# Kernel tuning notes

Measured on AMD Instinct MI355X. Metric: run time of the kernel, lower is better.

Reference implementation:

```python
import jax, jax.numpy as jnp
import numpy as np

THRESHOLD = 1.0
NEG_SLOPE = 0.2
N_NODES = 100000
N_EDGES = 1600000
DIM = 64
N_LAYERS = 3


def setup_inputs() -> dict:
    key = jax.random.key(0)
    ks = jax.random.split(key, 6)
    x = jax.random.normal(ks[0], (N_NODES, DIM), dtype=jnp.float32)
    edge_index = jax.random.randint(ks[1], (2, N_EDGES), 0, N_NODES, dtype=jnp.int64)
    scale = 1.0 / np.sqrt(DIM)
    W = jax.random.normal(ks[2], (N_LAYERS, DIM, DIM), dtype=jnp.float32) * scale
    a_src = jax.random.normal(ks[3], (N_LAYERS, DIM), dtype=jnp.float32) * scale
    a_dst = jax.random.normal(ks[4], (N_LAYERS, DIM), dtype=jnp.float32) * scale
    b = jnp.zeros((N_LAYERS, DIM), dtype=jnp.float32)
    return {"x": x, "edge_index": edge_index, "W": W, "a_src": a_src, "a_dst": a_dst, "b": b}


def reference(x, edge_index, W, a_src, a_dst, b):
    N = x.shape[0]
    # GATConv default add_self_loops=True: append (i -> i) for every node
    self_loop = jnp.arange(N, dtype=edge_index.dtype)
    src = jnp.concatenate([edge_index[0], self_loop])  # message source j
    dst = jnp.concatenate([edge_index[1], self_loop])  # message target i

    h = x
    for l in range(W.shape[0]):
        hw = h @ W[l]                       # [N, d] linear transform
        alpha_s = hw @ a_src[l]             # [N] per-node src attention logits
        alpha_d = hw @ a_dst[l]             # [N] per-node dst attention logits
        e = jax.nn.leaky_relu(alpha_s[src] + alpha_d[dst], NEG_SLOPE)  # [E']
        # softmax over incoming edges of each dst node (segment softmax)
        m = jax.ops.segment_max(e, dst, num_segments=N)
        p = jnp.exp(e - m[dst])
        s = jax.ops.segment_sum(p, dst, num_segments=N)
        attn = p / s[dst]
        out = jax.ops.segment_sum(attn[:, None] * hw[src], dst, num_segments=N)
        h = jnp.clip(out + b[l], -THRESHOLD, THRESHOLD)  # act_fn = clamp
    return h
```

## Files before the change

kernel.cpp:

```cpp
#include <hip/hip_runtime.h>
#include <hip/hip_fp16.h>

#define NN 100000
#define NE 1600000
#define DIM 64
#define NL 3
#define SLOPE 0.2f

#define BSH 9
#define NBUCK ((NN + 511) >> BSH)
#define EPT 16
#define TILE (256 * EPT)
#define MT 128

static __device__ __forceinline__ float lrelu(float x) { return x > 0.f ? x : SLOPE * x; }

static __device__ __forceinline__ float4 load_h4(const ushort* __restrict__ base, size_t off) {
    uint2 u = *(const uint2*)(base + off);
    __half2 h0 = __builtin_bit_cast(__half2, u.x);
    __half2 h1 = __builtin_bit_cast(__half2, u.y);
    float2 f0 = __half22float2(h0);
    float2 f1 = __half22float2(h1);
    return make_float4(f0.x, f0.y, f1.x, f1.y);
}


__global__ __launch_bounds__(256) void k_bucket_hist(const int* __restrict__ ei, int* __restrict__ bcnt) {
    __shared__ int h[256];
    int t = threadIdx.x;
    h[t] = 0;
    __syncthreads();
    for (int e = blockIdx.x * 256 + t; e < NE; e += 256 * 256) atomicAdd(&h[ei[NE + e] >> BSH], 1);
    __syncthreads();
    if (t < NBUCK && h[t]) atomicAdd(&bcnt[t], h[t]);
}

__global__ void k_bucket_scan(const int* __restrict__ bcnt, int* __restrict__ bbase, int* __restrict__ bcur,
                              int* __restrict__ offs) {
    __shared__ int sm[256];
    int t = threadIdx.x;
    sm[t] = (t < NBUCK) ? bcnt[t] : 0;
    __syncthreads();
    for (int off = 1; off < 256; off <<= 1) {
        int x = (t >= off) ? sm[t - off] : 0;
        __syncthreads();
        sm[t] += x;
        __syncthreads();
    }
    if (t < NBUCK) {
        int ex = (t == 0) ? 0 : sm[t - 1];
        bbase[t] = ex;
        bcur[t] = ex;
    }
    if (t == 0) {
        bbase[NBUCK] = NE;
        offs[NN] = NE;
    }
}

__global__ __launch_bounds__(256) void k_partition(const int* __restrict__ ei, int* __restrict__ bcur,
                                                   int2* __restrict__ pairs) {
    __shared__ int2 tile[TILE];
    __shared__ int cnt[256], ofsx[256], gdel[256], sm[256];
    int t = threadIdx.x;
    int ts = blockIdx.x * TILE;
    int tilecnt = NE - ts;
    if (tilecnt > TILE) tilecnt = TILE;
    cnt[t] = 0;
    __syncthreads();
    int srcv[EPT], dstv[EPT], rk[EPT];
#pragma unroll
    for (int k = 0; k < EPT; k++) {
        int e = ts + k * 256 + t;
        if (e < NE) {
            srcv[k] = ei[e];
            dstv[k] = ei[NE + e];
            rk[k] = atomicAdd(&cnt[dstv[k] >> BSH], 1);
        } else {
            rk[k] = -1;
        }
    }
    __syncthreads();
    sm[t] = cnt[t];
    __syncthreads();
    for (int off = 1; off < 256; off <<= 1) {
        int x = (t >= off) ? sm[t - off] : 0;
        __syncthreads();
        sm[t] += x;
        __syncthreads();
    }
    ofsx[t] = (t == 0) ? 0 : sm[t - 1];
    __syncthreads();
#pragma unroll
    for (int k = 0; k < EPT; k++) {
        if (rk[k] >= 0) tile[ofsx[dstv[k] >> BSH] + rk[k]] = make_int2(srcv[k], dstv[k]);
    }
    if (t < NBUCK && cnt[t]) gdel[t] = atomicAdd(&bcur[t], cnt[t]) - ofsx[t];
    __syncthreads();
    for (int i = t; i < tilecnt; i += 256) {
        int2 p = tile[i];
        pairs[gdel[p.y >> BSH] + i] = p;
    }
}

__global__ __launch_bounds__(256) void k_node_csr(const int2* __restrict__ pairs, const int* __restrict__ bbase,
                                                  int* __restrict__ offs, int* __restrict__ csr) {
    __shared__ int deg[512], sofs[512], scur[512], sm[256];
    int t = threadIdx.x;
    int b = blockIdx.x;
    int nodeBase = b << BSH;
    int nNodes = NN - nodeBase;
    if (nNodes > 512) nNodes = 512;
    deg[t] = 0;
    deg[t + 256] = 0;
    __syncthreads();
    int ebeg = bbase[b], eend = bbase[b + 1];
    for (int i = ebeg + t; i < eend; i += 256) atomicAdd(&deg[pairs[i].y - nodeBase], 1);
    __syncthreads();
    int a0 = deg[2 * t], a1 = deg[2 * t + 1];
    sm[t] = a0 + a1;
    __syncthreads();
    for (int off = 1; off < 256; off <<= 1) {
        int x = (t >= off) ? sm[t - off] : 0;
        __syncthreads();
        sm[t] += x;
        __syncthreads();
    }
    int base = (t == 0) ? 0 : sm[t - 1];
    sofs[2 * t] = base;
    sofs[2 * t + 1] = base + a0;
    scur[2 * t] = 0;
    scur[2 * t + 1] = 0;
    __syncthreads();
    for (int n = t; n < nNodes; n += 256) offs[nodeBase + n] = ebeg + sofs[n];
    for (int i = ebeg + t; i < eend; i += 256) {
        int2 p = pairs[i];
        int ln = p.y - nodeBase;
        int r = atomicAdd(&scur[ln], 1);
        csr[ebeg + sofs[ln] + r] = p.x;
    }
}


__global__ __launch_bounds__(256) void k_transform(const float* __restrict__ h, const float* __restrict__ W,
                                                   const float* __restrict__ avs, const float* __restrict__ avd,
                                                   ushort* __restrict__ hw, float* __restrict__ als,
                                                   float* __restrict__ ald) {
    __shared__ float sh[MT][65];
    __shared__ float sw[64][64];
    int t = threadIdx.x;
    int tx = t & 15, ty = t >> 4;
    int base = blockIdx.x * MT;
    int rows = NN - base;
    if (rows > MT) rows = MT;
    {
        const float4* Wv = (const float4*)W;
        float4* swv = (float4*)sw;
        for (int i = t; i < 1024; i += 256) swv[i] = Wv[i];
    }
    for (int i = t; i < MT * 16; i += 256) {
        int r = i >> 4, cs = i & 15;
        float4 v = (r < rows) ? *(const float4*)(h + (size_t)(base + r) * 64 + cs * 4)
                              : make_float4(0.f, 0.f, 0.f, 0.f);
        sh[r][cs * 4 + 0] = v.x;
        sh[r][cs * 4 + 1] = v.y;
        sh[r][cs * 4 + 2] = v.z;
        sh[r][cs * 4 + 3] = v.w;
    }
    __syncthreads();
    float acc[8][4] = {};
    int r0 = ty * 8;
#pragma unroll 4
    for (int k = 0; k < 64; k++) {
        float4 b = *(const float4*)(&sw[k][tx * 4]);
#pragma unroll
        for (int r = 0; r < 8; r++) {
            float a = sh[r0 + r][k];
            acc[r][0] = fmaf(a, b.x, acc[r][0]);
            acc[r][1] = fmaf(a, b.y, acc[r][1]);
            acc[r][2] = fmaf(a, b.z, acc[r][2]);
            acc[r][3] = fmaf(a, b.w, acc[r][3]);
        }
    }
    float4 as4 = *(const float4*)(avs + tx * 4);
    float4 ad4 = *(const float4*)(avd + tx * 4);
#pragma unroll
    for (int r = 0; r < 8; r++) {
        int row = r0 + r;
        bool ok = row < rows;
        if (ok) {
            __half2 h0 = __floats2half2_rn(acc[r][0], acc[r][1]);
            __half2 h1 = __floats2half2_rn(acc[r][2], acc[r][3]);
            uint2 u;
            u.x = __builtin_bit_cast(unsigned int, h0);
            u.y = __builtin_bit_cast(unsigned int, h1);
            *(uint2*)(hw + (size_t)(base + row) * 64 + tx * 4) = u;
        }
        float ps = acc[r][0] * as4.x + acc[r][1] * as4.y + acc[r][2] * as4.z + acc[r][3] * as4.w;
        float pd = acc[r][0] * ad4.x + acc[r][1] * ad4.y + acc[r][2] * ad4.z + acc[r][3] * ad4.w;
#pragma unroll
        for (int off = 1; off <= 8; off <<= 1) {
            ps += __shfl_xor(ps, off);
            pd += __shfl_xor(pd, off);
        }
        if (tx == 0 && ok) {
            als[base + row] = ps;
            ald[base + row] = pd;
        }
    }
}

__global__ __launch_bounds__(256) void k_aggregate(const ushort* __restrict__ hw, const float* __restrict__ als,
                                                   const float* __restrict__ ald, const int* __restrict__ offs,
                                                   const int* __restrict__ csr, const float* __restrict__ bv,
                                                   float* __restrict__ out) {
    int t = threadIdx.x, wave = t >> 6, lane = t & 63;
    int i = blockIdx.x * 4 + wave;
    if (i >= NN) return;
    int q = lane >> 4, c = lane & 15;
    float ad = ald[i];
    float eself = lrelu(als[i] + ad);
    float m = eself;
    float s = 0.f;
    float4 acc = make_float4(0.f, 0.f, 0.f, 0.f);
    int beg = offs[i], end = offs[i + 1];
    for (int cb = beg; cb < end; cb += 64) {
        int cnt = end - cb;
        if (cnt > 64) cnt = 64;
        int src = 0;
        float e = -1e30f;
        if (lane < cnt) {
            src = csr[cb + lane];
            e = lrelu(als[src] + ad);
        }
        float cm = e;
#pragma unroll
        for (int off = 32; off; off >>= 1) cm = fmaxf(cm, __shfl_xor(cm, off));
        float mn = fmaxf(m, cm);
        float p = (lane < cnt) ? __expf(e - mn) : 0.f;
        float cs = p;
#pragma unroll
        for (int off = 32; off; off >>= 1) cs += __shfl_xor(cs, off);
        float sc = __expf(m - mn);
        s = fmaf(s, sc, cs);
        acc.x *= sc;
        acc.y *= sc;
        acc.z *= sc;
        acc.w *= sc;
        m = mn;
        int steps = (cnt + 15) >> 4;
        for (int st = 0; st < steps; st++) {
            int jb = st * 16 + q;
            int s0 = __shfl(src, jb);
            int s1 = __shfl(src, jb + 4);
            int s2 = __shfl(src, jb + 8);
            int s3 = __shfl(src, jb + 12);
            float p0 = __shfl(p, jb);
            float p1 = __shfl(p, jb + 4);
            float p2 = __shfl(p, jb + 8);
            float p3 = __shfl(p, jb + 12);
            float4 v0 = load_h4(hw, (size_t)s0 * 64 + c * 4);
            float4 v1 = load_h4(hw, (size_t)s1 * 64 + c * 4);
            float4 v2 = load_h4(hw, (size_t)s2 * 64 + c * 4);
            float4 v3 = load_h4(hw, (size_t)s3 * 64 + c * 4);
            acc.x = fmaf(p0, v0.x, acc.x);
            acc.y = fmaf(p0, v0.y, acc.y);
            acc.z = fmaf(p0, v0.z, acc.z);
            acc.w = fmaf(p0, v0.w, acc.w);
            acc.x = fmaf(p1, v1.x, acc.x);
            acc.y = fmaf(p1, v1.y, acc.y);
            acc.z = fmaf(p1, v1.z, acc.z);
            acc.w = fmaf(p1, v1.w, acc.w);
            acc.x = fmaf(p2, v2.x, acc.x);
            acc.y = fmaf(p2, v2.y, acc.y);
            acc.z = fmaf(p2, v2.z, acc.z);
            acc.w = fmaf(p2, v2.w, acc.w);
            acc.x = fmaf(p3, v3.x, acc.x);
            acc.y = fmaf(p3, v3.y, acc.y);
            acc.z = fmaf(p3, v3.z, acc.z);
            acc.w = fmaf(p3, v3.w, acc.w);
        }
    }
#pragma unroll
    for (int off = 16; off <= 32; off <<= 1) {
        acc.x += __shfl_xor(acc.x, off);
        acc.y += __shfl_xor(acc.y, off);
        acc.z += __shfl_xor(acc.z, off);
        acc.w += __shfl_xor(acc.w, off);
    }
    float ps = __expf(eself - m);
    s += ps;
    float4 hv = load_h4(hw, (size_t)i * 64 + c * 4);
    acc.x = fmaf(ps, hv.x, acc.x);
    acc.y = fmaf(ps, hv.y, acc.y);
    acc.z = fmaf(ps, hv.z, acc.z);
    acc.w = fmaf(ps, hv.w, acc.w);
    float inv = 1.f / s;
    const float4 bq = *(const float4*)(bv + c * 4);
    float4 o;
    o.x = fminf(fmaxf(fmaf(acc.x, inv, bq.x), -1.f), 1.f);
    o.y = fminf(fmaxf(fmaf(acc.y, inv, bq.y), -1.f), 1.f);
    o.z = fminf(fmaxf(fmaf(acc.z, inv, bq.z), -1.f), 1.f);
    o.w = fminf(fmaxf(fmaf(acc.w, inv, bq.w), -1.f), 1.f);
    if (q == 0) *(float4*)(out + (size_t)i * 64 + c * 4) = o;
}


extern "C" void kernel_launch(void* const* d_in, const int* in_sizes, int n_in, void* d_out, int out_size,
                              void* d_ws, size_t ws_size, hipStream_t stream) {
    const float* x = (const float*)d_in[0];
    const int* ei = (const int*)d_in[1];
    const float* W = (const float*)d_in[2];
    const float* a_s = (const float*)d_in[3];
    const float* a_d = (const float*)d_in[4];
    const float* b = (const float*)d_in[5];
    float* out = (float*)d_out;

    char* w = (char*)d_ws;
    auto alloc = [&](size_t bytes) -> char* {
        char* p = w;
        w += (bytes + 255) & ~(size_t)255;
        return p;
    };
    int* bcnt = (int*)alloc(256 * 4);
    int* bbase = (int*)alloc(257 * 4);
    int* bcur = (int*)alloc(256 * 4);
    int* offs = (int*)alloc((NN + 1) * 4);
    int* csr = (int*)alloc((size_t)NE * 4);
    size_t layer_bytes = (size_t)(2 * NN) * 4 + (size_t)NN * DIM * 2;
    size_t build_bytes = (size_t)NE * 8;
    char* region = alloc(layer_bytes > build_bytes ? layer_bytes : build_bytes);
    int2* pairs = (int2*)region;
    float* als = (float*)region;
    float* ald = als + NN;
    ushort* hwb = (ushort*)(ald + NN);

    hipMemsetAsync(bcnt, 0, 256 * 4, stream);
    k_bucket_hist<<<256, 256, 0, stream>>>(ei, bcnt);
    k_bucket_scan<<<1, 256, 0, stream>>>(bcnt, bbase, bcur, offs);
    k_partition<<<(NE + TILE - 1) / TILE, 256, 0, stream>>>(ei, bcur, pairs);
    k_node_csr<<<NBUCK, 256, 0, stream>>>(pairs, bbase, offs, csr);

    const float* hin = x;
    for (int l = 0; l < NL; l++) {
        k_transform<<<(NN + MT - 1) / MT, 256, 0, stream>>>(hin, W + l * DIM * DIM, a_s + l * DIM, a_d + l * DIM,
                                                            hwb, als, ald);
        k_aggregate<<<(NN + 3) / 4, 256, 0, stream>>>(hwb, als, ald, offs, csr, b + l * DIM, out);
        hin = out;
    }
}
```

Before: 357.8 us.

## Rebuild CSR with global-atomic degree/scan/fill and map one 16-lane group per node

The per-bucket shared-memory CSR builder is replaced by separate global kernels: an atomic degree count, a three-stage prefix scan and an atomic fill. The aggregate kernel now gives each 16-lane group its own destination node, so a wave handles four nodes and needs no cross-group reduction at the end. The bucket histogram also reads destinations as int4 vectors. This trades the per-bucket locality of the old builder for more launches and global atomics. The fill order within each node becomes nondeterministic, which can change floating-point summation order.

```diff
diff --git a/kernel.cpp b/kernel.cpp
--- a/kernel.cpp
+++ b/kernel.cpp
@@ -30,13 +30,20 @@
     int t = threadIdx.x;
     h[t] = 0;
     __syncthreads();
-    for (int e = blockIdx.x * 256 + t; e < NE; e += 256 * 256) atomicAdd(&h[ei[NE + e] >> BSH], 1);
+    const int4* d4 = (const int4*)(ei + NE);
+    int idx = blockIdx.x * 256 + t;
+    if (idx < NE / 4) {
+        int4 v = d4[idx];
+        atomicAdd(&h[v.x >> BSH], 1);
+        atomicAdd(&h[v.y >> BSH], 1);
+        atomicAdd(&h[v.z >> BSH], 1);
+        atomicAdd(&h[v.w >> BSH], 1);
+    }
     __syncthreads();
     if (t < NBUCK && h[t]) atomicAdd(&bcnt[t], h[t]);
 }
 
-__global__ void k_bucket_scan(const int* __restrict__ bcnt, int* __restrict__ bbase, int* __restrict__ bcur,
-                              int* __restrict__ offs) {
+__global__ void k_bucket_scan(const int* __restrict__ bcnt, int* __restrict__ bbase, int* __restrict__ bcur) {
     __shared__ int sm[256];
     int t = threadIdx.x;
     sm[t] = (t < NBUCK) ? bcnt[t] : 0;
@@ -52,10 +59,7 @@
         bbase[t] = ex;
         bcur[t] = ex;
     }
-    if (t == 0) {
-        bbase[NBUCK] = NE;
-        offs[NN] = NE;
-    }
+    if (t == 0) bbase[NBUCK] = NE;
 }
 
 __global__ __launch_bounds__(256) void k_partition(const int* __restrict__ ei, int* __restrict__ bcur,
@@ -103,22 +107,26 @@
     }
 }
 
-__global__ __launch_bounds__(256) void k_node_csr(const int2* __restrict__ pairs, const int* __restrict__ bbase,
-                                                  int* __restrict__ offs, int* __restrict__ csr) {
-    __shared__ int deg[512], sofs[512], scur[512], sm[256];
-    int t = threadIdx.x;
-    int b = blockIdx.x;
-    int nodeBase = b << BSH;
-    int nNodes = NN - nodeBase;
-    if (nNodes > 512) nNodes = 512;
-    deg[t] = 0;
-    deg[t + 256] = 0;
-    __syncthreads();
-    int ebeg = bbase[b], eend = bbase[b + 1];
-    for (int i = ebeg + t; i < eend; i += 256) atomicAdd(&deg[pairs[i].y - nodeBase], 1);
-    __syncthreads();
-    int a0 = deg[2 * t], a1 = deg[2 * t + 1];
-    sm[t] = a0 + a1;
+__global__ __launch_bounds__(256) void k_deg(const int2* __restrict__ pairs, int* __restrict__ deg) {
+    int e = blockIdx.x * 256 + threadIdx.x;
+    if (e < NE) atomicAdd(&deg[pairs[e].y], 1);
+}
+
+__global__ __launch_bounds__(256) void k_scan1(const int* __restrict__ deg, int* __restrict__ part,
+                                               int* __restrict__ bsum) {
+    __shared__ int sm[256];
+    int t = threadIdx.x;
+    int base = blockIdx.x * 1024 + t * 4;
+    int v[4];
+    int run = 0;
+#pragma unroll
+    for (int j = 0; j < 4; j++) {
+        int idx = base + j;
+        int d = (idx < NN) ? deg[idx] : 0;
+        v[j] = run;
+        run += d;
+    }
+    sm[t] = run;
     __syncthreads();
     for (int off = 1; off < 256; off <<= 1) {
         int x = (t >= off) ? sm[t - off] : 0;
@@ -126,18 +134,47 @@
         sm[t] += x;
         __syncthreads();
     }
-    int base = (t == 0) ? 0 : sm[t - 1];
-    sofs[2 * t] = base;
-    sofs[2 * t + 1] = base + a0;
-    scur[2 * t] = 0;
-    scur[2 * t + 1] = 0;
-    __syncthreads();
-    for (int n = t; n < nNodes; n += 256) offs[nodeBase + n] = ebeg + sofs[n];
-    for (int i = ebeg + t; i < eend; i += 256) {
-        int2 p = pairs[i];
-        int ln = p.y - nodeBase;
-        int r = atomicAdd(&scur[ln], 1);
-        csr[ebeg + sofs[ln] + r] = p.x;
+    int ex = (t == 0) ? 0 : sm[t - 1];
+    if (t == 255) bsum[blockIdx.x] = sm[255];
+#pragma unroll
+    for (int j = 0; j < 4; j++) {
+        int idx = base + j;
+        if (idx < NN) part[idx] = ex + v[j];
+    }
+}
+
+__global__ void k_scan2(int* bsum, int nb) {
+    __shared__ int sm[256];
+    int t = threadIdx.x;
+    sm[t] = (t < nb) ? bsum[t] : 0;
+    __syncthreads();
+    for (int off = 1; off < 256; off <<= 1) {
+        int x = (t >= off) ? sm[t - off] : 0;
+        __syncthreads();
+        sm[t] += x;
+        __syncthreads();
+    }
+    if (t < nb) bsum[t] = (t == 0) ? 0 : sm[t - 1];
+}
+
+__global__ __launch_bounds__(256) void k_scan3(const int* __restrict__ part, const int* __restrict__ bsum,
+                                               int* __restrict__ offs, int* __restrict__ cur) {
+    int i = blockIdx.x * 256 + threadIdx.x;
+    if (i < NN) {
+        int o = part[i] + bsum[i >> 10];
+        offs[i] = o;
+        cur[i] = o;
+    }
+    if (i == NN) offs[NN] = NE;
+}
+
+__global__ __launch_bounds__(256) void k_fill(const int2* __restrict__ pairs, int* __restrict__ cur,
+                                              int* __restrict__ csr) {
+    int e = blockIdx.x * 256 + threadIdx.x;
+    if (e < NE) {
+        int2 p = pairs[e];
+        int pos = atomicAdd(&cur[p.y], 1);
+        csr[pos] = p.x;
     }
 }
 
@@ -215,32 +252,33 @@
                                                    const int* __restrict__ csr, const float* __restrict__ bv,
                                                    float* __restrict__ out) {
     int t = threadIdx.x, wave = t >> 6, lane = t & 63;
-    int i = blockIdx.x * 4 + wave;
+    int grp = lane >> 4, l = lane & 15;
+    int grpbase = grp << 4;
+    int i = blockIdx.x * 16 + wave * 4 + grp;
     if (i >= NN) return;
-    int q = lane >> 4, c = lane & 15;
     float ad = ald[i];
     float eself = lrelu(als[i] + ad);
     float m = eself;
     float s = 0.f;
     float4 acc = make_float4(0.f, 0.f, 0.f, 0.f);
     int beg = offs[i], end = offs[i + 1];
-    for (int cb = beg; cb < end; cb += 64) {
+    for (int cb = beg; cb < end; cb += 16) {
         int cnt = end - cb;
-        if (cnt > 64) cnt = 64;
+        if (cnt > 16) cnt = 16;
         int src = 0;
         float e = -1e30f;
-        if (lane < cnt) {
-            src = csr[cb + lane];
+        if (l < cnt) {
+            src = csr[cb + l];
             e = lrelu(als[src] + ad);
         }
         float cm = e;
 #pragma unroll
-        for (int off = 32; off; off >>= 1) cm = fmaxf(cm, __shfl_xor(cm, off));
+        for (int off = 1; off <= 8; off <<= 1) cm = fmaxf(cm, __shfl_xor(cm, off));
         float mn = fmaxf(m, cm);
-        float p = (lane < cnt) ? __expf(e - mn) : 0.f;
+        float p = (l < cnt) ? __expf(e - mn) : 0.f;
         float cs = p;
 #pragma unroll
-        for (int off = 32; off; off >>= 1) cs += __shfl_xor(cs, off);
+        for (int off = 1; off <= 8; off <<= 1) cs += __shfl_xor(cs, off);
         float sc = __expf(m - mn);
         s = fmaf(s, sc, cs);
         acc.x *= sc;
@@ -248,21 +286,21 @@
         acc.z *= sc;
         acc.w *= sc;
         m = mn;
-        int steps = (cnt + 15) >> 4;
-        for (int st = 0; st < steps; st++) {
-            int jb = st * 16 + q;
+        int iters = (cnt + 3) >> 2;
+        for (int j = 0; j < iters; j++) {
+            int jb = grpbase + j * 4;
             int s0 = __shfl(src, jb);
-            int s1 = __shfl(src, jb + 4);
-            int s2 = __shfl(src, jb + 8);
-            int s3 = __shfl(src, jb + 12);
+            int s1 = __shfl(src, jb + 1);
+            int s2 = __shfl(src, jb + 2);
+            int s3 = __shfl(src, jb + 3);
             float p0 = __shfl(p, jb);
-            float p1 = __shfl(p, jb + 4);
-            float p2 = __shfl(p, jb + 8);
-            float p3 = __shfl(p, jb + 12);
-            float4 v0 = load_h4(hw, (size_t)s0 * 64 + c * 4);
-            float4 v1 = load_h4(hw, (size_t)s1 * 64 + c * 4);
-            float4 v2 = load_h4(hw, (size_t)s2 * 64 + c * 4);
-            float4 v3 = load_h4(hw, (size_t)s3 * 64 + c * 4);
+            float p1 = __shfl(p, jb + 1);
+            float p2 = __shfl(p, jb + 2);
+            float p3 = __shfl(p, jb + 3);
+            float4 v0 = load_h4(hw, (size_t)s0 * 64 + l * 4);
+            float4 v1 = load_h4(hw, (size_t)s1 * 64 + l * 4);
+            float4 v2 = load_h4(hw, (size_t)s2 * 64 + l * 4);
+            float4 v3 = load_h4(hw, (size_t)s3 * 64 + l * 4);
             acc.x = fmaf(p0, v0.x, acc.x);
             acc.y = fmaf(p0, v0.y, acc.y);
             acc.z = fmaf(p0, v0.z, acc.z);
@@ -281,28 +319,21 @@
             acc.w = fmaf(p3, v3.w, acc.w);
         }
     }
-#pragma unroll
-    for (int off = 16; off <= 32; off <<= 1) {
-        acc.x += __shfl_xor(acc.x, off);
-        acc.y += __shfl_xor(acc.y, off);
-        acc.z += __shfl_xor(acc.z, off);
-        acc.w += __shfl_xor(acc.w, off);
-    }
     float ps = __expf(eself - m);
     s += ps;
-    float4 hv = load_h4(hw, (size_t)i * 64 + c * 4);
+    float4 hv = load_h4(hw, (size_t)i * 64 + l * 4);
     acc.x = fmaf(ps, hv.x, acc.x);
     acc.y = fmaf(ps, hv.y, acc.y);
     acc.z = fmaf(ps, hv.z, acc.z);
     acc.w = fmaf(ps, hv.w, acc.w);
     float inv = 1.f / s;
-    const float4 bq = *(const float4*)(bv + c * 4);
+    const float4 bq = *(const float4*)(bv + l * 4);
     float4 o;
     o.x = fminf(fmaxf(fmaf(acc.x, inv, bq.x), -1.f), 1.f);
     o.y = fminf(fmaxf(fmaf(acc.y, inv, bq.y), -1.f), 1.f);
     o.z = fminf(fmaxf(fmaf(acc.z, inv, bq.z), -1.f), 1.f);
     o.w = fminf(fmaxf(fmaf(acc.w, inv, bq.w), -1.f), 1.f);
-    if (q == 0) *(float4*)(out + (size_t)i * 64 + c * 4) = o;
+    *(float4*)(out + (size_t)i * 64 + l * 4) = o;
 }
 
 
@@ -326,6 +357,10 @@
     int* bbase = (int*)alloc(257 * 4);
     int* bcur = (int*)alloc(256 * 4);
     int* offs = (int*)alloc((NN + 1) * 4);
+    int* cur = (int*)alloc(NN * 4);
+    int* deg = (int*)alloc(NN * 4);
+    int* part = (int*)alloc(NN * 4);
+    int* bsum = (int*)alloc(1024);
     int* csr = (int*)alloc((size_t)NE * 4);
     size_t layer_bytes = (size_t)(2 * NN) * 4 + (size_t)NN * DIM * 2;
     size_t build_bytes = (size_t)NE * 8;
@@ -336,16 +371,22 @@
     ushort* hwb = (ushort*)(ald + NN);
 
     hipMemsetAsync(bcnt, 0, 256 * 4, stream);
-    k_bucket_hist<<<256, 256, 0, stream>>>(ei, bcnt);
-    k_bucket_scan<<<1, 256, 0, stream>>>(bcnt, bbase, bcur, offs);
+    hipMemsetAsync(deg, 0, NN * 4, stream);
+    k_bucket_hist<<<(NE / 4 + 255) / 256, 256, 0, stream>>>(ei, bcnt);
+    k_bucket_scan<<<1, 256, 0, stream>>>(bcnt, bbase, bcur);
     k_partition<<<(NE + TILE - 1) / TILE, 256, 0, stream>>>(ei, bcur, pairs);
-    k_node_csr<<<NBUCK, 256, 0, stream>>>(pairs, bbase, offs, csr);
+    k_deg<<<(NE + 255) / 256, 256, 0, stream>>>(pairs, deg);
+    int nb = (NN + 1023) / 1024;
+    k_scan1<<<nb, 256, 0, stream>>>(deg, part, bsum);
+    k_scan2<<<1, 256, 0, stream>>>(bsum, nb);
+    k_scan3<<<(NN + 1 + 255) / 256, 256, 0, stream>>>(part, bsum, offs, cur);
+    k_fill<<<(NE + 255) / 256, 256, 0, stream>>>(pairs, cur, csr);
 
     const float* hin = x;
     for (int l = 0; l < NL; l++) {
         k_transform<<<(NN + MT - 1) / MT, 256, 0, stream>>>(hin, W + l * DIM * DIM, a_s + l * DIM, a_d + l * DIM,
                                                             hwb, als, ald);
-        k_aggregate<<<(NN + 3) / 4, 256, 0, stream>>>(hwb, als, ald, offs, csr, b + l * DIM, out);
+        k_aggregate<<<(NN + 15) / 16, 256, 0, stream>>>(hwb, als, ald, offs, csr, b + l * DIM, out);
         hin = out;
     }
 }
```

Result: slower. 405.9 us (+13.5%).
